# Kernel optimization log

Measured on AMD Instinct MI355X. Metric: run time of the kernel, lower is better.

The kernel has to match this reference:

```python
import jax, jax.numpy as jnp
import numpy as np

N_E = 8192
E_DIM = 256
B = 32768


def setup_inputs() -> dict:
    key = jax.random.key(0)
    kz, ke = jax.random.split(key)
    z = jax.random.normal(kz, (B, E_DIM), dtype=jnp.float32)
    # matches nn.Embedding init: uniform(-1/n_e, 1/n_e)
    embedding = jax.random.uniform(ke, (N_E, E_DIM), dtype=jnp.float32,
                                   minval=-1.0 / N_E, maxval=1.0 / N_E)
    return {"z": z, "embedding": embedding}


def reference(z, embedding):
    # squared euclidean distances: [B, n_e]
    d = (jnp.sum(z * z, axis=1, keepdims=True)
         + jnp.sum(embedding * embedding, axis=1)
         - 2.0 * jnp.einsum('bd,nd->bn', z, embedding))
    min_encoding_indices = jnp.argmin(d, axis=1)          # [B] int
    z_q = embedding[min_encoding_indices]                 # [B, e_dim] gather
    return z_q, min_encoding_indices
```

## Files before the change

kernel.cpp:

```cpp
#include <hip/hip_runtime.h>

constexpr int NE = 8192;
constexpr int ED = 256;
constexpr int BS = 32768;
constexpr float DELTA = 4e-4f;

typedef short bf16x8 __attribute__((ext_vector_type(8)));
typedef float f32x4 __attribute__((ext_vector_type(4)));

constexpr size_t WSTR = (size_t)NE * 64;

#define GLOAD_LDS16(g, l) __builtin_amdgcn_global_load_lds( \
    (const __attribute__((address_space(1))) void*)(g),     \
    (__attribute__((address_space(3))) void*)(l), 16, 0, 0)

__device__ __forceinline__ short f2bf(float f) {
    unsigned u = __float_as_uint(f);
    u = u + 0x7FFFu + ((u >> 16) & 1u);
    return (short)(u >> 16);
}
__device__ __forceinline__ unsigned bf16_rd(float x) {
    unsigned u = __float_as_uint(x);
    unsigned h = u >> 16;
    if ((u & 0x80000000u) && (u & 0xFFFFu)) ++h;
    return h;
}
__device__ __forceinline__ unsigned umn(unsigned a, unsigned b) { return a < b ? a : b; }
__device__ __forceinline__ unsigned umx(unsigned a, unsigned b) { return a > b ? a : b; }
__device__ __forceinline__ unsigned med3(unsigned a, unsigned b, unsigned c) {
    unsigned r;
    asm("v_med3_u32 %0, %1, %2, %3" : "=v"(r) : "v"(a), "v"(b), "v"(c));
    return r;
}

__global__ void sq_np_kernel(const float* __restrict__ a, float* __restrict__ out) {
    int gtid = blockIdx.x * blockDim.x + threadIdx.x;
    int wave = gtid >> 6;
    int lane = threadIdx.x & 63;
    int sub  = lane & 7;
    int row  = wave * 8 + (lane >> 3);
    const float* p = a + (size_t)row * ED;
    float b0 = 0.f, b1 = 0.f;
#pragma unroll
    for (int t = 0; t < 16; ++t) { float v = p[8 * t + sub];       b0 = __fadd_rn(b0, __fmul_rn(v, v)); }
#pragma unroll
    for (int t = 0; t < 16; ++t) { float v = p[128 + 8 * t + sub]; b1 = __fadd_rn(b1, __fmul_rn(v, v)); }
    b0 = __fadd_rn(b0, __shfl_xor(b0, 1));
    b0 = __fadd_rn(b0, __shfl_xor(b0, 2));
    b0 = __fadd_rn(b0, __shfl_xor(b0, 4));
    b1 = __fadd_rn(b1, __shfl_xor(b1, 1));
    b1 = __fadd_rn(b1, __shfl_xor(b1, 2));
    b1 = __fadd_rn(b1, __shfl_xor(b1, 4));
    if (sub == 0) out[row] = __fadd_rn(b0, b1);
}

__global__ void cvt_ebT_kernel(const float* __restrict__ e, const float* __restrict__ e2,
                               char* __restrict__ ebT) {
    int i = blockIdx.x * blockDim.x + threadIdx.x;
    int c = i >> 5;
    int u = i & 31;
    int w = u >> 2, lg = u & 3;
    const float* p = e + (size_t)c * ED + w * 32 + lg * 8;
    float4 v0 = *reinterpret_cast<const float4*>(p);
    float4 v1 = *reinterpret_cast<const float4*>(p + 4);
    bf16x8 h;
    h[0] = f2bf(v0.x * -2.f); h[1] = f2bf(v0.y * -2.f);
    h[2] = f2bf(v0.z * -2.f); h[3] = f2bf(v0.w * -2.f);
    h[4] = f2bf(v1.x * -2.f); h[5] = f2bf(v1.y * -2.f);
    h[6] = f2bf(v1.z * -2.f); h[7] = f2bf(v1.w * -2.f);
    *reinterpret_cast<bf16x8*>(ebT + (size_t)w * WSTR + (size_t)c * 64 + lg * 16) = h;
    if (i < NE) {
        bf16x8 s0 = {};
        s0[0] = f2bf(e2[i]);
        s0[1] = f2bf(0.25f);
        bf16x8 zz = {};
        char* qp = ebT + 8 * WSTR + (size_t)i * 64;
        *reinterpret_cast<bf16x8*>(qp)      = s0;
        *reinterpret_cast<bf16x8*>(qp + 16) = zz;
        *reinterpret_cast<bf16x8*>(qp + 32) = zz;
        *reinterpret_cast<bf16x8*>(qp + 48) = zz;
    }
}

__global__ __launch_bounds__(256, 2) void vq_pass1(
        const float* __restrict__ z, const char* __restrict__ ebT,
        uint2* __restrict__ wsp) {
    __shared__ __align__(16) char Bs[2][32768];

    const int tid  = threadIdx.x;
    const int wid  = tid >> 6, lane = tid & 63;
    const int l15  = lane & 15, lg = lane >> 4;
    const int kblk = blockIdx.x;
    const int rg   = (kblk & 7) | ((kblk >> 5) << 3);
    const int q    = (kblk >> 3) & 3;
    const int c0q  = q * 2048;
    const int wr0  = rg * 256 + wid * 64;

    const char* gsrc[8];
#pragma unroll
    for (int it = 0; it < 8; ++it) {
        int L = it * 256 + tid;
        int c = L >> 5;
        int r = (L & 31) ^ (c & 7);
        gsrc[it] = ebT + (size_t)(r >> 2) * WSTR + (size_t)(c0q + c) * 64 + (r & 3) * 16;
    }
#pragma unroll
    for (int it = 0; it < 8; ++it)
        GLOAD_LDS16(gsrc[it], &Bs[0][(it * 256 + tid) * 16]);

    bf16x8 zreg[4][8];
#pragma unroll
    for (int j = 0; j < 4; ++j) {
        const float* zr = z + (size_t)(wr0 + j * 16 + l15) * ED + lg * 8;
#pragma unroll
        for (int t8 = 0; t8 < 8; ++t8) {
            float4 v0 = *reinterpret_cast<const float4*>(zr + t8 * 32);
            float4 v1 = *reinterpret_cast<const float4*>(zr + t8 * 32 + 4);
            bf16x8 h;
            h[0] = f2bf(v0.x); h[1] = f2bf(v0.y); h[2] = f2bf(v0.z); h[3] = f2bf(v0.w);
            h[4] = f2bf(v1.x); h[5] = f2bf(v1.y); h[6] = f2bf(v1.z); h[7] = f2bf(v1.w);
            zreg[j][t8] = h;
        }
    }
    bf16x8 zE = {};
    if (lg == 0) { zE[0] = (short)0x3F80; zE[1] = (short)0x4000; }

    const int hsh = (l15 & 7) << 4;
    int xw[8];
#pragma unroll
    for (int w = 0; w < 8; ++w) xw[w] = (w * 64 + lg * 16) ^ hsh;
    const char* ebase = ebT + (size_t)(c0q + l15) * 64 + lg * 16;

    bf16x8 bufE[2];
    unsigned rk1[4], rk2[4];

    for (int t = 0; t < 32; ++t) {
        __syncthreads();
        if (t < 31) {
#pragma unroll
            for (int it = 0; it < 8; ++it)
                GLOAD_LDS16(gsrc[it] + (size_t)(t + 1) * 4096,
                            &Bs[(t + 1) & 1][(it * 256 + tid) * 16]);
        }
        const char* B = Bs[t & 1];
        f32x4 acc[2][4];
#pragma unroll
        for (int s = 0; s < 8; ++s) {
            const int i0 = (s >> 2) * 2;
            if ((s & 3) == 0) {
#pragma unroll
                for (int i2 = 0; i2 < 2; ++i2)
#pragma unroll
                    for (int j = 0; j < 4; ++j) acc[i2][j] = (f32x4){0.f, 0.f, 0.f, 0.f};
                size_t colbyte = (size_t)((t << 6) + (i0 << 4)) << 6;
                bufE[0] = *reinterpret_cast<const bf16x8*>(ebase + 8 * WSTR + colbyte);
                bufE[1] = *reinterpret_cast<const bf16x8*>(ebase + 8 * WSTR + colbyte + 1024);
            }
            bf16x8 af[2][2];
#pragma unroll
            for (int i2 = 0; i2 < 2; ++i2)
#pragma unroll
                for (int tt = 0; tt < 2; ++tt)
                    af[i2][tt] = *reinterpret_cast<const bf16x8*>(
                        B + (size_t)((i0 + i2) * 16 + l15) * 512 + xw[(s & 3) * 2 + tt]);

            __builtin_amdgcn_s_setprio(1);
#pragma unroll
            for (int tt = 0; tt < 2; ++tt)
#pragma unroll
                for (int i2 = 0; i2 < 2; ++i2)
#pragma unroll
                    for (int j = 0; j < 4; ++j)
                        acc[i2][j] = __builtin_amdgcn_mfma_f32_16x16x32_bf16(
                            af[i2][tt], zreg[j][(s & 3) * 2 + tt],
                            acc[i2][j], 0, 0, 0);
            __builtin_amdgcn_s_setprio(0);

            if ((s & 3) == 3) {
                __builtin_amdgcn_s_setprio(1);
#pragma unroll
                for (int i2 = 0; i2 < 2; ++i2)
#pragma unroll
                    for (int j = 0; j < 4; ++j)
                        acc[i2][j] = __builtin_amdgcn_mfma_f32_16x16x32_bf16(
                            bufE[i2], zE, acc[i2][j], 0, 0, 0);
                __builtin_amdgcn_s_setprio(0);

                const unsigned cb = (unsigned)((t & 1) * 64 + lg * 4);
#pragma unroll
                for (int j = 0; j < 4; ++j) {
                    unsigned c1 = 0xFFFFFFFFu, c2 = 0xFFFFFFFFu;
#pragma unroll
                    for (int i2 = 0; i2 < 2; ++i2) {
#pragma unroll
                        for (int qq = 0; qq < 4; ++qq) {
                            unsigned k = (__float_as_uint(acc[i2][j][qq]) & 0xFFFFFF80u)
                                       | (cb + (i0 + i2) * 16 + qq);
                            c2 = med3(c1, c2, k);
                            c1 = umn(c1, k);
                        }
                    }
                    if (i0 == 0) {
                        if ((t & 1) == 0) { rk1[j] = c1; rk2[j] = c2; }
                        else {
                            unsigned mxh = umx(rk1[j], c1);
                            rk1[j] = umn(rk1[j], c1);
                            rk2[j] = umn(umn(rk2[j], c2), mxh);
                        }
                    } else {
                        unsigned mxh = umx(rk1[j], c1);
                        c1 = umn(rk1[j], c1);
                        c2 = umn(umn(rk2[j], c2), mxh);
                        if ((t & 1) == 0) {
                            rk1[j] = c1; rk2[j] = c2;
                        } else {
#pragma unroll
                            for (int off = 16; off < 64; off <<= 1) {
                                unsigned o1 = (unsigned)__shfl_xor((int)c1, off);
                                unsigned o2 = (unsigned)__shfl_xor((int)c2, off);
                                unsigned mx2 = umx(c1, o1);
                                c1 = umn(c1, o1);
                                c2 = umn(umn(c2, o2), mx2);
                            }
                            if (lg == 0) {
                                float m1f = __uint_as_float(c1 & 0xFFFFFF80u) - 0.5f;
                                float m2f = __uint_as_float(c2 & 0xFFFFFF80u) - 0.5f;
                                wsp[(size_t)(wr0 + j * 16 + l15) * 64 + (q * 16 + (t >> 1))] =
                                    make_uint2(__float_as_uint(m1f),
                                               (bf16_rd(m2f) << 16) | (c1 & 0x7Fu));
                            }
                        }
                    }
                }
            }
        }
    }
}

__global__ __launch_bounds__(256) void vq_pass2(
        const float* __restrict__ z, const float* __restrict__ e,
        const float* __restrict__ z2, const float* __restrict__ e2,
        const uint2* __restrict__ wsp, float* __restrict__ out) {
    __shared__ __align__(16) float zrow[4][ED];
    const int wid = threadIdx.x >> 6, lane = threadIdx.x & 63;
    const int r = blockIdx.x * 4 + wid;

    *reinterpret_cast<float4*>(&zrow[wid][lane * 4]) =
        *reinterpret_cast<const float4*>(z + (size_t)r * ED + lane * 4);
    __syncthreads();

    const float z2r = z2[r];
    uint2 p = wsp[(size_t)r * 64 + lane];
    float m1 = __uint_as_float(p.x);
    int   i8 = (int)(p.y & 0xFFu);
    float m2 = __uint_as_float(p.y & 0xFFFF0000u);

    float rmn = m1;
#pragma unroll
    for (int off = 1; off < 64; off <<= 1) rmn = fminf(rmn, __shfl_xor(rmn, off));
    const float thr = rmn + DELTA;

    const bool cF = (m2 <= thr);
    const bool cS = (m1 <= thr) && !cF;
    unsigned long long bS = __ballot(cS);
    unsigned long long bF = __ballot(cF);

    float bd = 3.4e38f;
    int   bc = NE;

    int myCol = -1;
    int cnt = 0;
    unsigned long long m = bS;
    while (true) {
        bool flush = (m == 0) || (cnt == 64);
        if (flush) {
            if (cnt > 0) {
                int ecol = (myCol >= 0) ? myCol : 0;
                const float* ec = e + (size_t)ecol * ED;
                float a0 = 0.f, a1 = 0.f, a2 = 0.f, a3 = 0.f;
#pragma unroll 8
                for (int t = 0; t < 64; ++t) {
                    float4 ev = *reinterpret_cast<const float4*>(ec + 4 * t);
                    float4 zv = *reinterpret_cast<const float4*>(&zrow[wid][4 * t]);
                    a0 = __fadd_rn(a0, __fmul_rn(zv.x, ev.x));
                    a1 = __fadd_rn(a1, __fmul_rn(zv.y, ev.y));
                    a2 = __fadd_rn(a2, __fmul_rn(zv.z, ev.z));
                    a3 = __fadd_rn(a3, __fmul_rn(zv.w, ev.w));
                }
                float s = __fadd_rn(__fadd_rn(a0, a1), __fadd_rn(a2, a3));
                float d = __fsub_rn(__fadd_rn(z2r, e2[ecol]), __fmul_rn(2.0f, s));
                if (myCol >= 0 && (d < bd || (d == bd && ecol < bc))) { bd = d; bc = ecol; }
                myCol = -1; cnt = 0;
            }
            if (m == 0) break;
        }
        int ch = __builtin_ctzll(m); m &= m - 1;
        int col = ch * 128 + __shfl(i8, ch);
        if (lane == cnt) myCol = col;
        ++cnt;
    }

    m = bF;
    while (m) {
        int ch = __builtin_ctzll(m); m &= m - 1;
#pragma unroll
        for (int hh = 0; hh < 2; ++hh) {
            int col = ch * 128 + hh * 64 + lane;
            const float* ec = e + (size_t)col * ED;
            float a0 = 0.f, a1 = 0.f, a2 = 0.f, a3 = 0.f;
#pragma unroll 8
            for (int t = 0; t < 64; ++t) {
                float4 ev = *reinterpret_cast<const float4*>(ec + 4 * t);
                float4 zv = *reinterpret_cast<const float4*>(&zrow[wid][4 * t]);
                a0 = __fadd_rn(a0, __fmul_rn(zv.x, ev.x));
                a1 = __fadd_rn(a1, __fmul_rn(zv.y, ev.y));
                a2 = __fadd_rn(a2, __fmul_rn(zv.z, ev.z));
                a3 = __fadd_rn(a3, __fmul_rn(zv.w, ev.w));
            }
            float s = __fadd_rn(__fadd_rn(a0, a1), __fadd_rn(a2, a3));
            float d = __fsub_rn(__fadd_rn(z2r, e2[col]), __fmul_rn(2.0f, s));
            if (d < bd || (d == bd && col < bc)) { bd = d; bc = col; }
        }
    }

#pragma unroll
    for (int off = 1; off < 64; off <<= 1) {
        float od = __shfl_xor(bd, off);
        int   oc = __shfl_xor(bc, off);
        if (od < bd || (od == bd && oc < bc)) { bd = od; bc = oc; }
    }
    if (lane == 0) out[(size_t)BS * ED + r] = (float)bc;
    *reinterpret_cast<float4*>(out + (size_t)r * ED + lane * 4) =
        *reinterpret_cast<const float4*>(e + (size_t)bc * ED + lane * 4);
}

extern "C" void kernel_launch(void* const* d_in, const int* in_sizes, int n_in,
                              void* d_out, int out_size, void* d_ws, size_t ws_size,
                              hipStream_t stream) {
    const float* z = (const float*)d_in[0];
    const float* e = (const float*)d_in[1];
    float* out   = (float*)d_out;
    float* e2np  = (float*)d_ws;
    float* z2np  = e2np + NE;
    uint2* wsp   = (uint2*)(z2np + BS);
    char*  ebT   = (char*)(wsp + (size_t)BS * 64);

    hipLaunchKernelGGL(sq_np_kernel, dim3(NE / 32), dim3(256), 0, stream, e, e2np);
    hipLaunchKernelGGL(sq_np_kernel, dim3(BS / 32), dim3(256), 0, stream, z, z2np);
    hipLaunchKernelGGL(cvt_ebT_kernel, dim3(NE * ED / 8 / 256), dim3(256), 0, stream,
                       e, e2np, ebT);
    hipLaunchKernelGGL(vq_pass1, dim3(512), dim3(256), 0, stream, z, ebT, wsp);
    hipLaunchKernelGGL(vq_pass2, dim3(BS / 4), dim3(256), 0, stream, z, e, z2np, e2np, wsp, out);
}
```

Baseline: 266.8 us.

## Split codebook into eighths with smaller LDS tiles and streaming top-2 tracking

Pass 1 now splits the codebook into 8 column chunks of 1024 instead of 4 of 2048, doubling the grid to 1024 blocks. Each iteration stages half as much data in LDS (16 KB per buffer), which may allow more blocks per CU. The top-2 selection now updates the running per-lane registers directly, using a fused and-or instruction, and reduces and writes once every four tiles. The aim is better occupancy and load balance. The cost is reloading z for twice as many blocks and doing more iterations per column with less work in each.

```diff
diff --git a/kernel.cpp b/kernel.cpp
--- a/kernel.cpp
+++ b/kernel.cpp
@@ -30,6 +30,11 @@
 __device__ __forceinline__ unsigned med3(unsigned a, unsigned b, unsigned c) {
     unsigned r;
     asm("v_med3_u32 %0, %1, %2, %3" : "=v"(r) : "v"(a), "v"(b), "v"(c));
+    return r;
+}
+__device__ __forceinline__ unsigned and_or(unsigned a, unsigned b, unsigned c) {
+    unsigned r;
+    asm("v_and_or_b32 %0, %1, %2, %3" : "=v"(r) : "v"(a), "v"(b), "v"(c));
     return r;
 }
 
@@ -85,27 +90,27 @@
 __global__ __launch_bounds__(256, 2) void vq_pass1(
         const float* __restrict__ z, const char* __restrict__ ebT,
         uint2* __restrict__ wsp) {
-    __shared__ __align__(16) char Bs[2][32768];
+    __shared__ __align__(16) char Bs[2][16384];
 
     const int tid  = threadIdx.x;
     const int wid  = tid >> 6, lane = tid & 63;
     const int l15  = lane & 15, lg = lane >> 4;
     const int kblk = blockIdx.x;
-    const int rg   = (kblk & 7) | ((kblk >> 5) << 3);
-    const int q    = (kblk >> 3) & 3;
-    const int c0q  = q * 2048;
+    const int rg   = (kblk & 7) | ((kblk >> 6) << 3);
+    const int q8   = (kblk >> 3) & 7;
+    const int c0q  = q8 * 1024;
     const int wr0  = rg * 256 + wid * 64;
 
-    const char* gsrc[8];
-#pragma unroll
-    for (int it = 0; it < 8; ++it) {
+    const char* gsrc[4];
+#pragma unroll
+    for (int it = 0; it < 4; ++it) {
         int L = it * 256 + tid;
         int c = L >> 5;
         int r = (L & 31) ^ (c & 7);
         gsrc[it] = ebT + (size_t)(r >> 2) * WSTR + (size_t)(c0q + c) * 64 + (r & 3) * 16;
     }
 #pragma unroll
-    for (int it = 0; it < 8; ++it)
+    for (int it = 0; it < 4; ++it)
         GLOAD_LDS16(gsrc[it], &Bs[0][(it * 256 + tid) * 16]);
 
     bf16x8 zreg[4][8];
@@ -133,26 +138,27 @@
 
     bf16x8 bufE[2];
     unsigned rk1[4], rk2[4];
+#pragma unroll
+    for (int j = 0; j < 4; ++j) { rk1[j] = 0xFFFFFFFFu; rk2[j] = 0xFFFFFFFFu; }
 
     for (int t = 0; t < 32; ++t) {
         __syncthreads();
         if (t < 31) {
 #pragma unroll
-            for (int it = 0; it < 8; ++it)
-                GLOAD_LDS16(gsrc[it] + (size_t)(t + 1) * 4096,
+            for (int it = 0; it < 4; ++it)
+                GLOAD_LDS16(gsrc[it] + (size_t)(t + 1) * 2048,
                             &Bs[(t + 1) & 1][(it * 256 + tid) * 16]);
         }
         const char* B = Bs[t & 1];
         f32x4 acc[2][4];
 #pragma unroll
-        for (int s = 0; s < 8; ++s) {
-            const int i0 = (s >> 2) * 2;
-            if ((s & 3) == 0) {
+        for (int s = 0; s < 4; ++s) {
+            if (s == 0) {
 #pragma unroll
                 for (int i2 = 0; i2 < 2; ++i2)
 #pragma unroll
                     for (int j = 0; j < 4; ++j) acc[i2][j] = (f32x4){0.f, 0.f, 0.f, 0.f};
-                size_t colbyte = (size_t)((t << 6) + (i0 << 4)) << 6;
+                size_t colbyte = (size_t)t << 11;
                 bufE[0] = *reinterpret_cast<const bf16x8*>(ebase + 8 * WSTR + colbyte);
                 bufE[1] = *reinterpret_cast<const bf16x8*>(ebase + 8 * WSTR + colbyte + 1024);
             }
@@ -162,7 +168,7 @@
 #pragma unroll
                 for (int tt = 0; tt < 2; ++tt)
                     af[i2][tt] = *reinterpret_cast<const bf16x8*>(
-                        B + (size_t)((i0 + i2) * 16 + l15) * 512 + xw[(s & 3) * 2 + tt]);
+                        B + (size_t)(i2 * 16 + l15) * 512 + xw[s * 2 + tt]);
 
             __builtin_amdgcn_s_setprio(1);
 #pragma unroll
@@ -172,11 +178,11 @@
 #pragma unroll
                     for (int j = 0; j < 4; ++j)
                         acc[i2][j] = __builtin_amdgcn_mfma_f32_16x16x32_bf16(
-                            af[i2][tt], zreg[j][(s & 3) * 2 + tt],
+                            af[i2][tt], zreg[j][s * 2 + tt],
                             acc[i2][j], 0, 0, 0);
             __builtin_amdgcn_s_setprio(0);
 
-            if ((s & 3) == 3) {
+            if (s == 3) {
                 __builtin_amdgcn_s_setprio(1);
 #pragma unroll
                 for (int i2 = 0; i2 < 2; ++i2)
@@ -186,50 +192,37 @@
                             bufE[i2], zE, acc[i2][j], 0, 0, 0);
                 __builtin_amdgcn_s_setprio(0);
 
-                const unsigned cb = (unsigned)((t & 1) * 64 + lg * 4);
+                const unsigned cb = (unsigned)((t & 3) * 32 + lg * 4);
 #pragma unroll
                 for (int j = 0; j < 4; ++j) {
-                    unsigned c1 = 0xFFFFFFFFu, c2 = 0xFFFFFFFFu;
 #pragma unroll
                     for (int i2 = 0; i2 < 2; ++i2) {
 #pragma unroll
                         for (int qq = 0; qq < 4; ++qq) {
-                            unsigned k = (__float_as_uint(acc[i2][j][qq]) & 0xFFFFFF80u)
-                                       | (cb + (i0 + i2) * 16 + qq);
-                            c2 = med3(c1, c2, k);
-                            c1 = umn(c1, k);
+                            unsigned k = and_or(__float_as_uint(acc[i2][j][qq]),
+                                                0xFFFFFF80u, cb + i2 * 16 + qq);
+                            rk2[j] = med3(rk1[j], rk2[j], k);
+                            rk1[j] = umn(rk1[j], k);
                         }
                     }
-                    if (i0 == 0) {
-                        if ((t & 1) == 0) { rk1[j] = c1; rk2[j] = c2; }
-                        else {
-                            unsigned mxh = umx(rk1[j], c1);
-                            rk1[j] = umn(rk1[j], c1);
-                            rk2[j] = umn(umn(rk2[j], c2), mxh);
+                    if ((t & 3) == 3) {
+                        unsigned c1 = rk1[j], c2 = rk2[j];
+#pragma unroll
+                        for (int off = 16; off < 64; off <<= 1) {
+                            unsigned o1 = (unsigned)__shfl_xor((int)c1, off);
+                            unsigned o2 = (unsigned)__shfl_xor((int)c2, off);
+                            unsigned mx2 = umx(c1, o1);
+                            c1 = umn(c1, o1);
+                            c2 = umn(umn(c2, o2), mx2);
                         }
-                    } else {
-                        unsigned mxh = umx(rk1[j], c1);
-                        c1 = umn(rk1[j], c1);
-                        c2 = umn(umn(rk2[j], c2), mxh);
-                        if ((t & 1) == 0) {
-                            rk1[j] = c1; rk2[j] = c2;
-                        } else {
-#pragma unroll
-                            for (int off = 16; off < 64; off <<= 1) {
-                                unsigned o1 = (unsigned)__shfl_xor((int)c1, off);
-                                unsigned o2 = (unsigned)__shfl_xor((int)c2, off);
-                                unsigned mx2 = umx(c1, o1);
-                                c1 = umn(c1, o1);
-                                c2 = umn(umn(c2, o2), mx2);
-                            }
-                            if (lg == 0) {
-                                float m1f = __uint_as_float(c1 & 0xFFFFFF80u) - 0.5f;
-                                float m2f = __uint_as_float(c2 & 0xFFFFFF80u) - 0.5f;
-                                wsp[(size_t)(wr0 + j * 16 + l15) * 64 + (q * 16 + (t >> 1))] =
-                                    make_uint2(__float_as_uint(m1f),
-                                               (bf16_rd(m2f) << 16) | (c1 & 0x7Fu));
-                            }
+                        if (lg == 0) {
+                            float m1f = __uint_as_float(c1 & 0xFFFFFF80u) - 0.5f;
+                            float m2f = __uint_as_float(c2 & 0xFFFFFF80u) - 0.5f;
+                            wsp[(size_t)(wr0 + j * 16 + l15) * 64 + (q8 * 8 + (t >> 2))] =
+                                make_uint2(__float_as_uint(m1f),
+                                           (bf16_rd(m2f) << 16) | (c1 & 0x7Fu));
                         }
+                        rk1[j] = 0xFFFFFFFFu; rk2[j] = 0xFFFFFFFFu;
                     }
                 }
             }
@@ -349,6 +342,6 @@
     hipLaunchKernelGGL(sq_np_kernel, dim3(BS / 32), dim3(256), 0, stream, z, z2np);
     hipLaunchKernelGGL(cvt_ebT_kernel, dim3(NE * ED / 8 / 256), dim3(256), 0, stream,
                        e, e2np, ebT);
-    hipLaunchKernelGGL(vq_pass1, dim3(512), dim3(256), 0, stream, z, ebT, wsp);
+    hipLaunchKernelGGL(vq_pass1, dim3(1024), dim3(256), 0, stream, z, ebT, wsp);
     hipLaunchKernelGGL(vq_pass2, dim3(BS / 4), dim3(256), 0, stream, z, e, z2np, e2np, wsp, out);
 }
```

New measurement: 278.1 us. +4.3%, slower.

## Add codebook norms in fp32 from LDS instead of extra MFMA, merge norm kernels

Applied to the files above, without the earlier changes.

The pass-1 GEMM no longer folds the e^2 term (plus a 0.25 offset) into the accumulators with an extra bf16 MFMA per tile. It now stages a precomputed fp32 e^2+0.5 array into LDS and adds it in fp32 before building the packed argmin key, using v_and_or_b32. The two squared-norm kernels are merged into one launch that also writes the offset array, and the conversion kernel drops its extra e^2 block. This trades 8 MFMAs per tile for 16 fp32 adds and an LDS read. It also changes the bias precision from bf16 to fp32 and the offset from 0.25 to 0.5, which may shift which candidates are kept.

```diff
diff --git a/kernel.cpp b/kernel.cpp
--- a/kernel.cpp
+++ b/kernel.cpp
@@ -32,14 +32,22 @@
     asm("v_med3_u32 %0, %1, %2, %3" : "=v"(r) : "v"(a), "v"(b), "v"(c));
     return r;
 }
-
-__global__ void sq_np_kernel(const float* __restrict__ a, float* __restrict__ out) {
+__device__ __forceinline__ unsigned and_or(unsigned a, unsigned b, unsigned c) {
+    unsigned r;
+    asm("v_and_or_b32 %0, %1, %2, %3" : "=v"(r) : "v"(a), "v"(b), "v"(c));
+    return r;
+}
+
+__global__ void sq_np_kernel(const float* __restrict__ z, const float* __restrict__ e,
+                             float* __restrict__ z2, float* __restrict__ e2,
+                             float* __restrict__ e2p5) {
     int gtid = blockIdx.x * blockDim.x + threadIdx.x;
     int wave = gtid >> 6;
     int lane = threadIdx.x & 63;
     int sub  = lane & 7;
     int row  = wave * 8 + (lane >> 3);
-    const float* p = a + (size_t)row * ED;
+    const float* p = (row < BS) ? (z + (size_t)row * ED)
+                                : (e + (size_t)(row - BS) * ED);
     float b0 = 0.f, b1 = 0.f;
 #pragma unroll
     for (int t = 0; t < 16; ++t) { float v = p[8 * t + sub];       b0 = __fadd_rn(b0, __fmul_rn(v, v)); }
@@ -51,11 +59,18 @@
     b1 = __fadd_rn(b1, __shfl_xor(b1, 1));
     b1 = __fadd_rn(b1, __shfl_xor(b1, 2));
     b1 = __fadd_rn(b1, __shfl_xor(b1, 4));
-    if (sub == 0) out[row] = __fadd_rn(b0, b1);
-}
-
-__global__ void cvt_ebT_kernel(const float* __restrict__ e, const float* __restrict__ e2,
-                               char* __restrict__ ebT) {
+    float tot = __fadd_rn(b0, b1);
+    if (sub == 0) {
+        if (row < BS) {
+            z2[row] = tot;
+        } else {
+            e2[row - BS]   = tot;
+            e2p5[row - BS] = tot + 0.5f;
+        }
+    }
+}
+
+__global__ void cvt_ebT_kernel(const float* __restrict__ e, char* __restrict__ ebT) {
     int i = blockIdx.x * blockDim.x + threadIdx.x;
     int c = i >> 5;
     int u = i & 31;
@@ -69,23 +84,13 @@
     h[4] = f2bf(v1.x * -2.f); h[5] = f2bf(v1.y * -2.f);
     h[6] = f2bf(v1.z * -2.f); h[7] = f2bf(v1.w * -2.f);
     *reinterpret_cast<bf16x8*>(ebT + (size_t)w * WSTR + (size_t)c * 64 + lg * 16) = h;
-    if (i < NE) {
-        bf16x8 s0 = {};
-        s0[0] = f2bf(e2[i]);
-        s0[1] = f2bf(0.25f);
-        bf16x8 zz = {};
-        char* qp = ebT + 8 * WSTR + (size_t)i * 64;
-        *reinterpret_cast<bf16x8*>(qp)      = s0;
-        *reinterpret_cast<bf16x8*>(qp + 16) = zz;
-        *reinterpret_cast<bf16x8*>(qp + 32) = zz;
-        *reinterpret_cast<bf16x8*>(qp + 48) = zz;
-    }
 }
 
 __global__ __launch_bounds__(256, 2) void vq_pass1(
         const float* __restrict__ z, const char* __restrict__ ebT,
-        uint2* __restrict__ wsp) {
+        const float* __restrict__ e2p5, uint2* __restrict__ wsp) {
     __shared__ __align__(16) char Bs[2][32768];
+    __shared__ float e2L[2048];
 
     const int tid  = threadIdx.x;
     const int wid  = tid >> 6, lane = tid & 63;
@@ -108,6 +113,13 @@
     for (int it = 0; it < 8; ++it)
         GLOAD_LDS16(gsrc[it], &Bs[0][(it * 256 + tid) * 16]);
 
+    {
+        float4 ea = *reinterpret_cast<const float4*>(e2p5 + c0q + tid * 8);
+        float4 eb = *reinterpret_cast<const float4*>(e2p5 + c0q + tid * 8 + 4);
+        *reinterpret_cast<float4*>(&e2L[tid * 8])     = ea;
+        *reinterpret_cast<float4*>(&e2L[tid * 8 + 4]) = eb;
+    }
+
     bf16x8 zreg[4][8];
 #pragma unroll
     for (int j = 0; j < 4; ++j) {
@@ -122,16 +134,12 @@
             zreg[j][t8] = h;
         }
     }
-    bf16x8 zE = {};
-    if (lg == 0) { zE[0] = (short)0x3F80; zE[1] = (short)0x4000; }
 
     const int hsh = (l15 & 7) << 4;
     int xw[8];
 #pragma unroll
     for (int w = 0; w < 8; ++w) xw[w] = (w * 64 + lg * 16) ^ hsh;
-    const char* ebase = ebT + (size_t)(c0q + l15) * 64 + lg * 16;
-
-    bf16x8 bufE[2];
+
     unsigned rk1[4], rk2[4];
 
     for (int t = 0; t < 32; ++t) {
@@ -152,9 +160,6 @@
                 for (int i2 = 0; i2 < 2; ++i2)
 #pragma unroll
                     for (int j = 0; j < 4; ++j) acc[i2][j] = (f32x4){0.f, 0.f, 0.f, 0.f};
-                size_t colbyte = (size_t)((t << 6) + (i0 << 4)) << 6;
-                bufE[0] = *reinterpret_cast<const bf16x8*>(ebase + 8 * WSTR + colbyte);
-                bufE[1] = *reinterpret_cast<const bf16x8*>(ebase + 8 * WSTR + colbyte + 1024);
             }
             bf16x8 af[2][2];
 #pragma unroll
@@ -177,14 +182,11 @@
             __builtin_amdgcn_s_setprio(0);
 
             if ((s & 3) == 3) {
-                __builtin_amdgcn_s_setprio(1);
+                f32x4 e2v[2];
 #pragma unroll
                 for (int i2 = 0; i2 < 2; ++i2)
-#pragma unroll
-                    for (int j = 0; j < 4; ++j)
-                        acc[i2][j] = __builtin_amdgcn_mfma_f32_16x16x32_bf16(
-                            bufE[i2], zE, acc[i2][j], 0, 0, 0);
-                __builtin_amdgcn_s_setprio(0);
+                    e2v[i2] = *reinterpret_cast<const f32x4*>(
+                        &e2L[t * 64 + (i0 + i2) * 16 + lg * 4]);
 
                 const unsigned cb = (unsigned)((t & 1) * 64 + lg * 4);
 #pragma unroll
@@ -194,8 +196,9 @@
                     for (int i2 = 0; i2 < 2; ++i2) {
 #pragma unroll
                         for (int qq = 0; qq < 4; ++qq) {
-                            unsigned k = (__float_as_uint(acc[i2][j][qq]) & 0xFFFFFF80u)
-                                       | (cb + (i0 + i2) * 16 + qq);
+                            float v = __fadd_rn(acc[i2][j][qq], e2v[i2][qq]);
+                            unsigned k = and_or(__float_as_uint(v), 0xFFFFFF80u,
+                                                cb + (i0 + i2) * 16 + qq);
                             c2 = med3(c1, c2, k);
                             c1 = umn(c1, k);
                         }
@@ -341,14 +344,15 @@
     const float* e = (const float*)d_in[1];
     float* out   = (float*)d_out;
     float* e2np  = (float*)d_ws;
-    float* z2np  = e2np + NE;
+    float* e2p5  = e2np + NE;
+    float* z2np  = e2p5 + NE;
     uint2* wsp   = (uint2*)(z2np + BS);
     char*  ebT   = (char*)(wsp + (size_t)BS * 64);
 
-    hipLaunchKernelGGL(sq_np_kernel, dim3(NE / 32), dim3(256), 0, stream, e, e2np);
-    hipLaunchKernelGGL(sq_np_kernel, dim3(BS / 32), dim3(256), 0, stream, z, z2np);
+    hipLaunchKernelGGL(sq_np_kernel, dim3((BS + NE) / 32), dim3(256), 0, stream,
+                       z, e, z2np, e2np, e2p5);
     hipLaunchKernelGGL(cvt_ebT_kernel, dim3(NE * ED / 8 / 256), dim3(256), 0, stream,
-                       e, e2np, ebT);
-    hipLaunchKernelGGL(vq_pass1, dim3(512), dim3(256), 0, stream, z, ebT, wsp);
+                       e, ebT);
+    hipLaunchKernelGGL(vq_pass1, dim3(512), dim3(256), 0, stream, z, ebT, e2p5, wsp);
     hipLaunchKernelGGL(vq_pass2, dim3(BS / 4), dim3(256), 0, stream, z, e, z2np, e2np, wsp, out);
 }
```

Result: faster. 259.0 us (-2.9%).
